# Kernel tuning notes

Hardware: AMD Instinct MI355X
Metric: run time of the kernel (lower is better)

## Reference

```python
import jax, jax.numpy as jnp
import numpy as np

# Block sizes (DGL message-flow-graph / sampled blocks)
NS0, ND0, NE0 = 300000, 50000, 800000   # block0: 2-hop frontier -> 1-hop frontier
NS1, ND1, NE1 = 50000, 8192, 131072     # block1: 1-hop frontier -> seed nodes


def _graph_conv(x, src, dst, ew, W, b, n_src, n_dst, weight_first):
    """DGL GraphConv with norm='both' and edge_weight.

    x: [n_src, d_in] source-node features; (src, dst): edge endpoints;
    ew: [E] edge weights. Degrees are UNWEIGHTED (copy of DGL semantics),
    clamped to >= 1. Weight applied before aggregation iff d_in > d_out.
    """
    ones_e = jnp.ones_like(ew)
    out_deg = jnp.clip(jax.ops.segment_sum(ones_e, src, num_segments=n_src), 1.0, None)
    h = x * (out_deg ** -0.5)[:, None]
    if weight_first:
        h = h @ W
    # gather-weight-scatter: m_v = sum_{e: e->v} ew_e * h_{src_e}
    msg = jax.ops.segment_sum(ew[:, None] * h[src], dst, num_segments=n_dst)
    in_deg = jnp.clip(jax.ops.segment_sum(ones_e, dst, num_segments=n_dst), 1.0, None)
    msg = msg * (in_deg ** -0.5)[:, None]
    if not weight_first:
        msg = msg @ W
    return msg + b


def setup_inputs() -> dict:
    key = jax.random.key(0)
    ks = jax.random.split(key, 12)
    in_f, hid_f, out_f = 256, 128, 128
    return {
        "x": jax.random.normal(ks[0], (NS0, in_f), dtype=jnp.float32),
        "src0": jax.random.randint(ks[1], (NE0,), 0, NS0, dtype=jnp.int64 if jax.config.jax_enable_x64 else jnp.int32).astype(jnp.int32),
        "dst0": jax.random.randint(ks[2], (NE0,), 0, ND0).astype(jnp.int32),
        "ew0": jax.random.normal(ks[3], (NE0,), dtype=jnp.float32),
        "src1": jax.random.randint(ks[4], (NE1,), 0, NS1).astype(jnp.int32),
        "dst1": jax.random.randint(ks[5], (NE1,), 0, ND1).astype(jnp.int32),
        "ew1": jax.random.normal(ks[6], (NE1,), dtype=jnp.float32),
        "W1": jax.random.normal(ks[7], (in_f, hid_f), dtype=jnp.float32) * 0.05,
        "b1": jax.random.normal(ks[8], (hid_f,), dtype=jnp.float32) * 0.05,
        "W2": jax.random.normal(ks[9], (hid_f, out_f), dtype=jnp.float32) * 0.05,
        "b2": jax.random.normal(ks[10], (out_f,), dtype=jnp.float32) * 0.05,
    }


def reference(x, src0, dst0, ew0, src1, dst1, ew1, W1, b1, W2, b2):
    # layer 1: in(256) > hidden(128) -> weight applied before aggregation
    h = jax.nn.relu(_graph_conv(x, src0, dst0, ew0, W1, b1, NS0, ND0, weight_first=True))
    # layer 2: hidden(128) <= out(128) -> aggregate then weight
    out = jax.nn.relu(_graph_conv(h, src1, dst1, ew1, W2, b2, NS1, ND1, weight_first=False))
    return out  # [ND1, out_f]
```

## Files before the change

### kernel.cpp

```cpp
#include <hip/hip_runtime.h>

#define NS0 300000
#define ND0 50000
#define NE0 800000
#define NS1 50000
#define ND1 8192
#define NE1 131072
#define IN_F 256
#define HID_F 128
#define SLOTS 64
#define NT16 (NS0 / 16)
#define GEMM_GRID 2048
#define BUILD_GRID 512

typedef __attribute__((ext_vector_type(8))) _Float16 half8_t;
typedef __attribute__((ext_vector_type(4))) float f32x4;

#define OFF_OUTDEG0I 0
#define OFF_OUTDEG1I 300000
#define OFF_CNT0     350000
#define OFF_CNT1     400000
#define ZERO_WORDS   408192
#define OFF_EDGE0    408192
#define OFF_EDGE1    6808192
#define OFF_H1       7856768
#define OFF_W1T      14256768
#define OFF_G        14273152

__global__ __launch_bounds__(256) void k_init(
    int4* __restrict__ p, const float* __restrict__ W1,
    _Float16* __restrict__ w1t) {
  if (blockIdx.x < 128) {
    int i = blockIdx.x * 256 + threadIdx.x;
    for (; i < ZERO_WORDS / 4; i += 128 * 256) p[i] = make_int4(0, 0, 0, 0);
  } else {
    int i = (blockIdx.x - 128) * 256 + threadIdx.x;
    for (; i < IN_F * HID_F; i += 32 * 256) {
      int k = i >> 7, n = i & 127;
      w1t[n * 256 + k] = (_Float16)W1[i];
    }
  }
}

#define LDB(p, o) (*reinterpret_cast<const half8_t*>((p) + (o)))
__global__ __launch_bounds__(256) void k_gemm_build(
    const float* __restrict__ x, const _Float16* __restrict__ w1t,
    _Float16* __restrict__ g,
    const int* __restrict__ src0, const int* __restrict__ dst0,
    const float* __restrict__ ew0, int* __restrict__ outdeg0,
    int* __restrict__ cnt0, int2* __restrict__ edge0,
    const int* __restrict__ src1, const int* __restrict__ dst1,
    const float* __restrict__ ew1, int* __restrict__ outdeg1,
    int* __restrict__ cnt1, int2* __restrict__ edge1) {
  __shared__ __align__(16) float ldsA[2][16 * 256];
  __shared__ _Float16 ldsT[4][16 * 40];

  if (blockIdx.x < BUILD_GRID) {
    int tid = blockIdx.x * 256 + threadIdx.x;
    int stride = BUILD_GRID * 256;
    for (int i = tid; i < NE0; i += stride) {
      int s = src0[i];
      int d = dst0[i];
      float w = ew0[i];
      atomicAdd(&outdeg0[s], 1);
      int slot = atomicAdd(&cnt0[d], 1);
      if (slot < SLOTS) edge0[d * SLOTS + slot] = make_int2(s, __float_as_int(w));
    }
    for (int i = tid; i < NE1; i += stride) {
      int s = src1[i];
      int d = dst1[i];
      float w = ew1[i];
      atomicAdd(&outdeg1[s], 1);
      int slot = atomicAdd(&cnt1[d], 1);
      if (slot < SLOTS) edge1[d * SLOTS + slot] = make_int2(s, __float_as_int(w));
    }
    return;
  }

  const int tid = threadIdx.x;
  const int wv = tid >> 6;
  const int lane = tid & 63;
  const int m = lane & 15;
  const int grp = lane >> 4;
  _Float16* tp = ldsT[wv];
  const int row_r = lane >> 2;
  const int q_r   = lane & 3;

  const _Float16* wb0 = w1t + (size_t)(32 * wv + m) * 256 + grp * 8;
  const _Float16* wb1 = wb0 + 16 * 256;
  const half8_t b00 = LDB(wb0, 0),   b01 = LDB(wb0, 32),  b02 = LDB(wb0, 64),
                b03 = LDB(wb0, 96),  b04 = LDB(wb0, 128), b05 = LDB(wb0, 160),
                b06 = LDB(wb0, 192), b07 = LDB(wb0, 224);
  const half8_t b10 = LDB(wb1, 0),   b11 = LDB(wb1, 32),  b12 = LDB(wb1, 64),
                b13 = LDB(wb1, 96),  b14 = LDB(wb1, 128), b15 = LDB(wb1, 160),
                b16 = LDB(wb1, 192), b17 = LDB(wb1, 224);

  const int bid = blockIdx.x - BUILD_GRID;

#define STAGE(BUFI, T)                                                         \
  {                                                                            \
    const float* tb = x + (size_t)(T) * 4096;                                  \
    _Pragma("unroll") for (int r = 0; r < 4; ++r) {                            \
      const int mr = wv * 4 + r;                                               \
      const float* srcp = tb + mr * 256 + ((lane ^ (mr & 7)) << 2);            \
      __builtin_amdgcn_global_load_lds(                                        \
          (const __attribute__((address_space(1))) unsigned int*)srcp,         \
          (__attribute__((address_space(3))) unsigned int*)&ldsA[BUFI][mr * 256], \
          16, 0, 0);                                                           \
    }                                                                          \
  }

#define STEP(BUFI, KB, B0, B1)                                                 \
  {                                                                            \
    const int c0 = ((KB * 8 + grp * 2) ^ (m & 7)) << 2;                        \
    const int c1 = ((KB * 8 + grp * 2 + 1) ^ (m & 7)) << 2;                    \
    const f32x4 fa = *reinterpret_cast<const f32x4*>(&ldsA[BUFI][m * 256 + c0]); \
    const f32x4 fb = *reinterpret_cast<const f32x4*>(&ldsA[BUFI][m * 256 + c1]); \
    half8_t af;                                                                \
    af[0] = (_Float16)fa[0]; af[1] = (_Float16)fa[1];                          \
    af[2] = (_Float16)fa[2]; af[3] = (_Float16)fa[3];                          \
    af[4] = (_Float16)fb[0]; af[5] = (_Float16)fb[1];                          \
    af[6] = (_Float16)fb[2]; af[7] = (_Float16)fb[3];                          \
    acc0 = __builtin_amdgcn_mfma_f32_16x16x32_f16(af, B0, acc0, 0, 0, 0);      \
    acc1 = __builtin_amdgcn_mfma_f32_16x16x32_f16(af, B1, acc1, 0, 0, 0);      \
  }

  STAGE(0, bid);
  __syncthreads();

  int cur = 0;
  for (int t = bid; t < NT16; t += GEMM_GRID) {
    const int nxt = t + GEMM_GRID;
    if (nxt < NT16) STAGE(cur ^ 1, nxt);
    {
      f32x4 acc0 = {0.f, 0.f, 0.f, 0.f};
      f32x4 acc1 = {0.f, 0.f, 0.f, 0.f};
      STEP(cur, 0, b00, b10)
      STEP(cur, 1, b01, b11)
      STEP(cur, 2, b02, b12)
      STEP(cur, 3, b03, b13)
      STEP(cur, 4, b04, b14)
      STEP(cur, 5, b05, b15)
      STEP(cur, 6, b06, b16)
      STEP(cur, 7, b07, b17)
#pragma unroll
      for (int r = 0; r < 4; ++r) {
        tp[(4 * grp + r) * 40 + m]      = (_Float16)acc0[r];
        tp[(4 * grp + r) * 40 + 16 + m] = (_Float16)acc1[r];
      }
      const half8_t ov =
          *reinterpret_cast<const half8_t*>(tp + row_r * 40 + q_r * 8);
      *reinterpret_cast<half8_t*>(
          g + ((size_t)t * 16 + row_r) * 128 + 32 * wv + q_r * 8) = ov;
    }
    __syncthreads();
    cur ^= 1;
  }
#undef STAGE
#undef STEP
}

__global__ __launch_bounds__(256) void k_gather1(
    const _Float16* __restrict__ g, const int* __restrict__ cnt,
    const int2* __restrict__ edge, const int* __restrict__ outdeg0,
    const int* __restrict__ outdeg1, const float* __restrict__ b1,
    float* __restrict__ h1) {
  const int w = (blockIdx.x * 256 + threadIdx.x) >> 6;
  const int lane = threadIdx.x & 63;
  const int gp = lane >> 4;
  const int sl = lane & 15;
  if (w >= ND0) return;
  const int deg = min(cnt[w], SLOTS);
  const int2* ep = edge + (size_t)w * SLOTS;
  float acc[8] = {0.f, 0.f, 0.f, 0.f, 0.f, 0.f, 0.f, 0.f};
  for (int e = 0; e < deg; e += 4) {
    const int idx = e + gp;
    int2 p = make_int2(0, 0);
    float c = 0.f;
    if (idx < deg) {
      p = ep[idx];
      c = __int_as_float(p.y) * rsqrtf(fmaxf((float)outdeg0[p.x], 1.0f));
    }
    const half8_t v =
        *reinterpret_cast<const half8_t*>(g + (size_t)p.x * 128 + sl * 8);
#pragma unroll
    for (int j = 0; j < 8; ++j) acc[j] = fmaf(c, (float)v[j], acc[j]);
  }
#pragma unroll
  for (int j = 0; j < 8; ++j) {
    acc[j] += __shfl_xor(acc[j], 16, 64);
    acc[j] += __shfl_xor(acc[j], 32, 64);
  }
  if (gp == 0) {
    const float sc = rsqrtf(fmaxf((float)deg, 1.0f));
    const float s1 = rsqrtf(fmaxf((float)outdeg1[w], 1.0f));
    const float4 bv0 = *reinterpret_cast<const float4*>(b1 + sl * 8);
    const float4 bv1 = *reinterpret_cast<const float4*>(b1 + sl * 8 + 4);
    float4 o0, o1;
    o0.x = fmaxf(fmaf(acc[0], sc, bv0.x), 0.0f) * s1;
    o0.y = fmaxf(fmaf(acc[1], sc, bv0.y), 0.0f) * s1;
    o0.z = fmaxf(fmaf(acc[2], sc, bv0.z), 0.0f) * s1;
    o0.w = fmaxf(fmaf(acc[3], sc, bv0.w), 0.0f) * s1;
    o1.x = fmaxf(fmaf(acc[4], sc, bv1.x), 0.0f) * s1;
    o1.y = fmaxf(fmaf(acc[5], sc, bv1.y), 0.0f) * s1;
    o1.z = fmaxf(fmaf(acc[6], sc, bv1.z), 0.0f) * s1;
    o1.w = fmaxf(fmaf(acc[7], sc, bv1.w), 0.0f) * s1;
    float* hr = h1 + (size_t)w * 128 + sl * 8;
    *reinterpret_cast<float4*>(hr) = o0;
    *reinterpret_cast<float4*>(hr + 4) = o1;
  }
}

#define FMA2(acc, c, v)        \
  acc.x = fmaf(c, v.x, acc.x); \
  acc.y = fmaf(c, v.y, acc.y);

__global__ __launch_bounds__(256) void k_layer2(
    const float* __restrict__ h1, const int* __restrict__ cnt,
    const int2* __restrict__ edge, const float* __restrict__ W2,
    const float* __restrict__ b2, float* __restrict__ out) {
  __shared__ float arow[8][HID_F];
  const int t = blockIdx.x;
  const int wv = threadIdx.x >> 6;
  const int lane = threadIdx.x & 63;

#pragma unroll
  for (int rr = 0; rr < 2; ++rr) {
    const int row = t * 8 + wv * 2 + rr;
    const int deg = min(cnt[row], SLOTS);
    const int2* ep = edge + (size_t)row * SLOTS;
    float2 acc = make_float2(0.f, 0.f);
    int e = 0;
    for (; e + 4 <= deg; e += 4) {
      int4 q0 = *reinterpret_cast<const int4*>(ep + e);
      int4 q1 = *reinterpret_cast<const int4*>(ep + e + 2);
      float2 v0 = *reinterpret_cast<const float2*>(h1 + (size_t)q0.x * HID_F + lane * 2);
      float2 v1 = *reinterpret_cast<const float2*>(h1 + (size_t)q0.z * HID_F + lane * 2);
      float2 v2 = *reinterpret_cast<const float2*>(h1 + (size_t)q1.x * HID_F + lane * 2);
      float2 v3 = *reinterpret_cast<const float2*>(h1 + (size_t)q1.z * HID_F + lane * 2);
      FMA2(acc, __int_as_float(q0.y), v0);
      FMA2(acc, __int_as_float(q0.w), v1);
      FMA2(acc, __int_as_float(q1.y), v2);
      FMA2(acc, __int_as_float(q1.w), v3);
    }
    for (; e < deg; ++e) {
      int2 p = ep[e];
      float2 v = *reinterpret_cast<const float2*>(h1 + (size_t)p.x * HID_F + lane * 2);
      FMA2(acc, __int_as_float(p.y), v);
    }
    const float sc = rsqrtf(fmaxf((float)deg, 1.0f));
    *reinterpret_cast<float2*>(&arow[wv * 2 + rr][lane * 2]) =
        make_float2(acc.x * sc, acc.y * sc);
  }
  __syncthreads();

  const int j = threadIdx.x & 127;
  const int rg = threadIdx.x >> 7;
  float a0 = 0.f, a1 = 0.f, a2 = 0.f, a3 = 0.f;
  const float* wj = W2 + j;
#pragma unroll 8
  for (int k = 0; k < HID_F; ++k) {
    const float wvv = wj[(size_t)k * 128];
    a0 = fmaf(arow[rg * 4 + 0][k], wvv, a0);
    a1 = fmaf(arow[rg * 4 + 1][k], wvv, a1);
    a2 = fmaf(arow[rg * 4 + 2][k], wvv, a2);
    a3 = fmaf(arow[rg * 4 + 3][k], wvv, a3);
  }
  const float bj = b2[j];
  const int row0 = t * 8 + rg * 4;
  out[(size_t)(row0 + 0) * 128 + j] = fmaxf(a0 + bj, 0.0f);
  out[(size_t)(row0 + 1) * 128 + j] = fmaxf(a1 + bj, 0.0f);
  out[(size_t)(row0 + 2) * 128 + j] = fmaxf(a2 + bj, 0.0f);
  out[(size_t)(row0 + 3) * 128 + j] = fmaxf(a3 + bj, 0.0f);
}

extern "C" void kernel_launch(void* const* d_in, const int* in_sizes, int n_in,
                              void* d_out, int out_size, void* d_ws, size_t ws_size,
                              hipStream_t stream) {
  const float* x    = (const float*)d_in[0];
  const int*   src0 = (const int*)d_in[1];
  const int*   dst0 = (const int*)d_in[2];
  const float* ew0  = (const float*)d_in[3];
  const int*   src1 = (const int*)d_in[4];
  const int*   dst1 = (const int*)d_in[5];
  const float* ew1  = (const float*)d_in[6];
  const float* W1   = (const float*)d_in[7];
  const float* b1   = (const float*)d_in[8];
  const float* W2   = (const float*)d_in[9];
  const float* b2   = (const float*)d_in[10];
  float* out = (float*)d_out;

  int*   wsi = (int*)d_ws;
  float* wsf = (float*)d_ws;
  int* outdeg0 = wsi + OFF_OUTDEG0I;
  int* outdeg1 = wsi + OFF_OUTDEG1I;
  int* cnt0    = wsi + OFF_CNT0;
  int* cnt1    = wsi + OFF_CNT1;
  int2* edge0  = (int2*)(wsi + OFF_EDGE0);
  int2* edge1  = (int2*)(wsi + OFF_EDGE1);
  float* h1    = wsf + OFF_H1;
  _Float16* w1t = (_Float16*)(wsi + OFF_W1T);
  _Float16* g   = (_Float16*)(wsi + OFF_G);

  k_init<<<160, 256, 0, stream>>>((int4*)d_ws, W1, w1t);
  k_gemm_build<<<BUILD_GRID + GEMM_GRID, 256, 0, stream>>>(
      x, w1t, g, src0, dst0, ew0, outdeg0, cnt0, edge0,
      src1, dst1, ew1, outdeg1, cnt1, edge1);
  k_gather1<<<(ND0 * 64) / 256, 256, 0, stream>>>(g, cnt0, edge0, outdeg0,
                                                  outdeg1, b1, h1);
  k_layer2<<<ND1 / 8, 256, 0, stream>>>(h1, cnt1, edge1, W2, b2, out);
}
```

Before: 226.9 us.

## Triple-buffer the x-tile LDS staging in the fused GEMM with explicit vmcnt waits

Replaces the double-buffered global_load_lds pipeline in the layer-1 GEMM with a three-stage ring buffer, so two future tiles are in flight while the current one is computed. Waits use explicit s_waitcnt vmcnt counts computed from outstanding stages and global stores, with raw s_barrier and sched_barrier in place of __syncthreads. The aim is to hide more global-load latency on the memory-bound x stream. In exchange LDS use grows by 16 KB per block, which may cut occupancy, and hand-counted vmcnt values risk races if the instruction count assumptions are wrong.

Result: slower. 244.0 us (+7.5%).

```diff
diff --git a/kernel.cpp b/kernel.cpp
--- a/kernel.cpp
+++ b/kernel.cpp
@@ -52,7 +52,7 @@
     const int* __restrict__ src1, const int* __restrict__ dst1,
     const float* __restrict__ ew1, int* __restrict__ outdeg1,
     int* __restrict__ cnt1, int2* __restrict__ edge1) {
-  __shared__ __align__(16) float ldsA[2][16 * 256];
+  __shared__ __align__(16) float ldsA[3][16 * 256];
   __shared__ _Float16 ldsT[4][16 * 40];
 
   if (blockIdx.x < BUILD_GRID) {
@@ -100,22 +100,23 @@
 #define STAGE(BUFI, T)                                                         \
   {                                                                            \
     const float* tb = x + (size_t)(T) * 4096;                                  \
+    float* lb = &ldsA[BUFI][0];                                                \
     _Pragma("unroll") for (int r = 0; r < 4; ++r) {                            \
       const int mr = wv * 4 + r;                                               \
       const float* srcp = tb + mr * 256 + ((lane ^ (mr & 7)) << 2);            \
       __builtin_amdgcn_global_load_lds(                                        \
           (const __attribute__((address_space(1))) unsigned int*)srcp,         \
-          (__attribute__((address_space(3))) unsigned int*)&ldsA[BUFI][mr * 256], \
+          (__attribute__((address_space(3))) unsigned int*)(lb + mr * 256),    \
           16, 0, 0);                                                           \
     }                                                                          \
   }
 
-#define STEP(BUFI, KB, B0, B1)                                                 \
+#define STEP(LB, KB, B0, B1)                                                   \
   {                                                                            \
     const int c0 = ((KB * 8 + grp * 2) ^ (m & 7)) << 2;                        \
     const int c1 = ((KB * 8 + grp * 2 + 1) ^ (m & 7)) << 2;                    \
-    const f32x4 fa = *reinterpret_cast<const f32x4*>(&ldsA[BUFI][m * 256 + c0]); \
-    const f32x4 fb = *reinterpret_cast<const f32x4*>(&ldsA[BUFI][m * 256 + c1]); \
+    const f32x4 fa = *reinterpret_cast<const f32x4*>(LB + m * 256 + c0);       \
+    const f32x4 fb = *reinterpret_cast<const f32x4*>(LB + m * 256 + c1);       \
     half8_t af;                                                                \
     af[0] = (_Float16)fa[0]; af[1] = (_Float16)fa[1];                          \
     af[2] = (_Float16)fa[2]; af[3] = (_Float16)fa[3];                          \
@@ -125,24 +126,46 @@
     acc1 = __builtin_amdgcn_mfma_f32_16x16x32_f16(af, B1, acc1, 0, 0, 0);      \
   }
 
-  STAGE(0, bid);
-  __syncthreads();
-
-  int cur = 0;
-  for (int t = bid; t < NT16; t += GEMM_GRID) {
-    const int nxt = t + GEMM_GRID;
-    if (nxt < NT16) STAGE(cur ^ 1, nxt);
+#define WAITP(P)                                                               \
+  do {                                                                         \
+    switch (P) {                                                               \
+      case 0: asm volatile("s_waitcnt vmcnt(0)"); break;                       \
+      case 1: asm volatile("s_waitcnt vmcnt(1)"); break;                       \
+      case 2: asm volatile("s_waitcnt vmcnt(2)"); break;                       \
+      case 4: asm volatile("s_waitcnt vmcnt(4)"); break;                       \
+      case 5: asm volatile("s_waitcnt vmcnt(5)"); break;                       \
+      case 6: asm volatile("s_waitcnt vmcnt(6)"); break;                       \
+      case 8: asm volatile("s_waitcnt vmcnt(8)"); break;                       \
+      case 9: asm volatile("s_waitcnt vmcnt(9)"); break;                       \
+      default: asm volatile("s_waitcnt vmcnt(10)"); break;                     \
+    }                                                                          \
+    __builtin_amdgcn_sched_barrier(0);                                         \
+  } while (0)
+
+  const int NTM = (NT16 - 1 - bid) / GEMM_GRID + 1;
+  int stages = (NTM < 3) ? NTM : 3;
+  for (int j = 0; j < stages; ++j) STAGE(j, bid + j * GEMM_GRID);
+
+  for (int i = 0; i < NTM; ++i) {
+    const int t = bid + i * GEMM_GRID;
+    const int buf = i % 3;
+    const int ns_after = stages - (i + 1);
+    const int st_after = (i < 2) ? i : 2;
+    WAITP(4 * ns_after + st_after);
+    __builtin_amdgcn_s_barrier();
+    __builtin_amdgcn_sched_barrier(0);
     {
+      const float* LB = &ldsA[buf][0];
       f32x4 acc0 = {0.f, 0.f, 0.f, 0.f};
       f32x4 acc1 = {0.f, 0.f, 0.f, 0.f};
-      STEP(cur, 0, b00, b10)
-      STEP(cur, 1, b01, b11)
-      STEP(cur, 2, b02, b12)
-      STEP(cur, 3, b03, b13)
-      STEP(cur, 4, b04, b14)
-      STEP(cur, 5, b05, b15)
-      STEP(cur, 6, b06, b16)
-      STEP(cur, 7, b07, b17)
+      STEP(LB, 0, b00, b10)
+      STEP(LB, 1, b01, b11)
+      STEP(LB, 2, b02, b12)
+      STEP(LB, 3, b03, b13)
+      STEP(LB, 4, b04, b14)
+      STEP(LB, 5, b05, b15)
+      STEP(LB, 6, b06, b16)
+      STEP(LB, 7, b07, b17)
 #pragma unroll
       for (int r = 0; r < 4; ++r) {
         tp[(4 * grp + r) * 40 + m]      = (_Float16)acc0[r];
@@ -153,11 +176,18 @@
       *reinterpret_cast<half8_t*>(
           g + ((size_t)t * 16 + row_r) * 128 + 32 * wv + q_r * 8) = ov;
     }
-    __syncthreads();
-    cur ^= 1;
+    __builtin_amdgcn_sched_barrier(0);
+    __builtin_amdgcn_s_barrier();
+    __builtin_amdgcn_sched_barrier(0);
+    const int tn = t + 3 * GEMM_GRID;
+    if (tn < NT16) {
+      STAGE(buf, tn);
+      ++stages;
+    }
   }
 #undef STAGE
 #undef STEP
+#undef WAITP
 }
 
 __global__ __launch_bounds__(256) void k_gather1(
```
